# Kernel tuning notes

Hardware: AMD Instinct MI355X
Metric: run time of the kernel (lower is better)

## Reference

```python
import jax, jax.numpy as jnp
import numpy as np
import math

M, DIN, DTGT = 65536, 256, 256   # feature count and feature dims
S, SD_IN, SD_TGT = 64, 256, 256  # num_slots, in_slot_dim, tgt_slot_dim
ITERS = 3
H_IN = 128                        # mlp_in hidden (hardcoded 128 in source)
H_TGT = SD_TGT if SD_TGT > 128 else 128  # mlp_tgt hidden

ARGS = ["inputs", "target", "in_slots", "tgt_slots",
        "ln_in_g", "ln_in_b", "ln_tgt_g", "ln_tgt_b",
        "Wk", "bk", "Wv", "bv", "Wvt", "bvt",
        "ln_slots_g", "ln_slots_b", "Wq", "bq",
        "gru_in_Wih", "gru_in_Whh", "gru_in_bih", "gru_in_bhh",
        "gru_tgt_Wih", "gru_tgt_Whh", "gru_tgt_bih", "gru_tgt_bhh",
        "ln_mi_g", "ln_mi_b", "mi_W1", "mi_b1", "mi_W2", "mi_b2",
        "ln_mt_g", "ln_mt_b", "mt_W1", "mt_b1", "mt_W2", "mt_b2"]


def _ln(x, g, b):
    m = jnp.mean(x, axis=-1, keepdims=True)
    v = jnp.var(x, axis=-1, keepdims=True)
    return (x - m) * jax.lax.rsqrt(v + 1e-5) * g + b


def _gru(x, h, Wih, Whh, bih, bhh):
    # torch.nn.GRUCell semantics; Wih: (D, 3H), Whh: (H, 3H)
    H = h.shape[-1]
    gi = x @ Wih + bih
    gh = h @ Whh + bhh
    r = jax.nn.sigmoid(gi[:, :H] + gh[:, :H])
    z = jax.nn.sigmoid(gi[:, H:2 * H] + gh[:, H:2 * H])
    n = jnp.tanh(gi[:, 2 * H:] + r * gh[:, 2 * H:])
    return (1.0 - z) * n + z * h


def _forward(inputs, target, in_slots, tgt_slots,
             ln_in_g, ln_in_b, ln_tgt_g, ln_tgt_b,
             Wk, bk, Wv, bv, Wvt, bvt,
             ln_slots_g, ln_slots_b, Wq, bq,
             gru_in_Wih, gru_in_Whh, gru_in_bih, gru_in_bhh,
             gru_tgt_Wih, gru_tgt_Whh, gru_tgt_bih, gru_tgt_bhh,
             ln_mi_g, ln_mi_b, mi_W1, mi_b1, mi_W2, mi_b2,
             ln_mt_g, ln_mt_b, mt_W1, mt_b1, mt_W2, mt_b2):
    inputs_norm = _ln(inputs, ln_in_g, ln_in_b)          # [M, DIN]
    in_k = inputs_norm @ Wk + bk                          # [M, SD_IN]
    in_v = inputs_norm @ Wv + bv                          # [M, SD_IN]
    tgt_v = _ln(target, ln_tgt_g, ln_tgt_b) @ Wvt + bvt   # [M, SD_TGT]
    scale = 1.0 / math.sqrt(in_k.shape[1])
    attn = None
    for _ in range(ITERS):
        q = _ln(in_slots, ln_slots_g, ln_slots_b) @ Wq + bq   # [S, SD_IN]
        logits = (q @ in_k.T) * scale                          # [S, M]
        attn = jax.nn.softmax(logits, axis=0)                  # softmax over SLOTS (dim=0)
        in_up = attn @ in_v                                    # [S, SD_IN]
        tgt_up = attn @ tgt_v                                  # [S, SD_TGT]
        in_slots = _gru(in_up, in_slots, gru_in_Wih, gru_in_Whh, gru_in_bih, gru_in_bhh)
        tgt_slots = _gru(tgt_up, tgt_slots, gru_tgt_Wih, gru_tgt_Whh, gru_tgt_bih, gru_tgt_bhh)
        in_slots = in_slots + (jax.nn.relu(_ln(in_slots, ln_mi_g, ln_mi_b) @ mi_W1 + mi_b1) @ mi_W2 + mi_b2)
        tgt_slots = tgt_slots + (jax.nn.relu(_ln(tgt_slots, ln_mt_g, ln_mt_b) @ mt_W1 + mt_b1) @ mt_W2 + mt_b2)
    return (in_slots, tgt_slots, attn)


def setup_inputs() -> dict:
    key = jax.random.key(0)
    ks = iter(jax.random.split(key, 64))
    rn = lambda shape, s=1.0: jax.random.normal(next(ks), shape, dtype=jnp.float32) * s
    w = 0.02
    d = {
        "inputs": rn((M, DIN)),
        "target": rn((M, DTGT)),
        "in_slots": rn((S, SD_IN)),
        "tgt_slots": rn((S, SD_TGT)),
        "ln_in_g": jnp.ones((DIN,)), "ln_in_b": jnp.zeros((DIN,)),
        "ln_tgt_g": jnp.ones((DTGT,)), "ln_tgt_b": jnp.zeros((DTGT,)),
        "Wk": rn((DIN, SD_IN), w), "bk": jnp.zeros((SD_IN,)),
        "Wv": rn((DIN, SD_IN), w), "bv": jnp.zeros((SD_IN,)),
        "Wvt": rn((DTGT, SD_TGT), w), "bvt": jnp.zeros((SD_TGT,)),
        "ln_slots_g": jnp.ones((SD_IN,)), "ln_slots_b": jnp.zeros((SD_IN,)),
        "Wq": rn((SD_IN, SD_IN), w), "bq": jnp.zeros((SD_IN,)),
        "gru_in_Wih": rn((SD_IN, 3 * SD_IN), w), "gru_in_Whh": rn((SD_IN, 3 * SD_IN), w),
        "gru_in_bih": jnp.zeros((3 * SD_IN,)), "gru_in_bhh": jnp.zeros((3 * SD_IN,)),
        "gru_tgt_Wih": rn((SD_TGT, 3 * SD_TGT), w), "gru_tgt_Whh": rn((SD_TGT, 3 * SD_TGT), w),
        "gru_tgt_bih": jnp.zeros((3 * SD_TGT,)), "gru_tgt_bhh": jnp.zeros((3 * SD_TGT,)),
        "ln_mi_g": jnp.ones((SD_IN,)), "ln_mi_b": jnp.zeros((SD_IN,)),
        "mi_W1": rn((SD_IN, H_IN), w), "mi_b1": jnp.zeros((H_IN,)),
        "mi_W2": rn((H_IN, SD_IN), w), "mi_b2": jnp.zeros((SD_IN,)),
        "ln_mt_g": jnp.ones((SD_TGT,)), "ln_mt_b": jnp.zeros((SD_TGT,)),
        "mt_W1": rn((SD_TGT, H_TGT), w), "mt_b1": jnp.zeros((H_TGT,)),
        "mt_W2": rn((H_TGT, SD_TGT), w), "mt_b2": jnp.zeros((SD_TGT,)),
    }
    return {k: d[k] for k in ARGS}


def reference(inputs, target, in_slots, tgt_slots,
              ln_in_g, ln_in_b, ln_tgt_g, ln_tgt_b,
              Wk, bk, Wv, bv, Wvt, bvt,
              ln_slots_g, ln_slots_b, Wq, bq,
              gru_in_Wih, gru_in_Whh, gru_in_bih, gru_in_bhh,
              gru_tgt_Wih, gru_tgt_Whh, gru_tgt_bih, gru_tgt_bhh,
              ln_mi_g, ln_mi_b, mi_W1, mi_b1, mi_W2, mi_b2,
              ln_mt_g, ln_mt_b, mt_W1, mt_b1, mt_W2, mt_b2):
    return _forward(inputs, target, in_slots, tgt_slots,
                    ln_in_g, ln_in_b, ln_tgt_g, ln_tgt_b,
                    Wk, bk, Wv, bv, Wvt, bvt,
                    ln_slots_g, ln_slots_b, Wq, bq,
                    gru_in_Wih, gru_in_Whh, gru_in_bih, gru_in_bhh,
                    gru_tgt_Wih, gru_tgt_Whh, gru_tgt_bih, gru_tgt_bhh,
                    ln_mi_g, ln_mi_b, mi_W1, mi_b1, mi_W2, mi_b2,
                    ln_mt_g, ln_mt_b, mt_W1, mt_b1, mt_W2, mt_b2)
```

## Files before the change

kernel.cpp:

```cpp
#include <hip/hip_runtime.h>
#include <hip/hip_bf16.h>
#include <math.h>

typedef __bf16 bf16_t;
typedef __bf16 bf16x8 __attribute__((ext_vector_type(8)));
typedef __bf16 bf16x4 __attribute__((ext_vector_type(4)));
typedef float f32x4 __attribute__((ext_vector_type(4)));

#define DEVI __device__ __forceinline__

DEVI f32x4 mfma16(bf16x8 a, bf16x8 b, f32x4 c) {
  return __builtin_amdgcn_mfma_f32_16x16x32_bf16(a, b, c, 0, 0, 0);
}
DEVI bf16x8 ld8(const bf16_t* p) { return *reinterpret_cast<const bf16x8*>(p); }


struct WtArgs { const float* s0; const float* s1; const float* s2; const float* s3;
                const float* s4; const float* s5; const float* s6; const float* s7;
                const float* s8; const float* s9; const float* s10; const float* s11; };

__global__ __launch_bounds__(256) void k_wtrans(WtArgs A, bf16_t* __restrict__ wt,
                                                const float* __restrict__ g_in,
                                                const float* __restrict__ g_tgt) {
  constexpr int offs[12] = {0,65536,131072,196608,262144,458752,655360,851968,
                            1048576,1081344,1114112,1179648};
  constexpr int Ks[12]   = {256,256,256,256,256,256,256,256,256,128,256,256};
  constexpr int Ns[12]   = {256,256,256,256,768,768,768,768,128,256,256,256};
  const int m = blockIdx.y;
  const int K = Ks[m], N = Ns[m];
  const int tn = N >> 6;
  const int tile = blockIdx.x;
  if (tile >= (K >> 6) * tn) return;
  const int tk = tile / tn, tc = tile - tk * tn;
  const float* sp;
  switch (m) {
    case 0: sp = A.s0; break; case 1: sp = A.s1; break; case 2: sp = A.s2; break;
    case 3: sp = A.s3; break; case 4: sp = A.s4; break; case 5: sp = A.s5; break;
    case 6: sp = A.s6; break; case 7: sp = A.s7; break; case 8: sp = A.s8; break;
    case 9: sp = A.s9; break; case 10: sp = A.s10; break; default: sp = A.s11; break;
  }
  const float* gv = (m == 2) ? g_tgt : ((m < 2) ? g_in : nullptr);
  __shared__ float ts[64][65];
  const int t = threadIdx.x;
  const int k0 = tk * 64, n0 = tc * 64;
  {
    const int c = t & 63, rq = t >> 6;
    #pragma unroll
    for (int i = 0; i < 16; ++i) {
      const int r = rq * 16 + i;
      float val = sp[(size_t)(k0 + r) * N + n0 + c];
      if (gv) val *= gv[k0 + r];
      ts[r][c] = val;
    }
  }
  __syncthreads();
  bf16_t* dst = wt + offs[m];
  const int n_l = t & 63, kq = t >> 6;
  #pragma unroll
  for (int h = 0; h < 2; ++h) {
    const int k_l = kq * 16 + h * 8;
    bf16x8 pk;
    #pragma unroll
    for (int e = 0; e < 8; ++e) pk[e] = (bf16_t)ts[k_l + e][n_l];
    const int n_g = n0 + n_l, k_g = k0 + k_l;
    const int nt = n_g >> 4, kc = k_g >> 5;
    const int lane = (((k_g >> 3) & 3) << 4) + (n_g & 15);
    *reinterpret_cast<bf16x8*>(dst + (((size_t)(nt * (K >> 5) + kc)) << 9) + lane * 8) = pk;
  }
}

__global__ __launch_bounds__(256) void k_bias(
    const float* __restrict__ Wk, const float* __restrict__ Wv, const float* __restrict__ Wvt,
    const float* __restrict__ b_in, const float* __restrict__ b_tgt,
    const float* __restrict__ bk, const float* __restrict__ bv, const float* __restrict__ bvt,
    float* __restrict__ out) {
  const int which = blockIdx.x;
  const float* W = which == 0 ? Wk : (which == 1 ? Wv : Wvt);
  const float* bvec = which == 2 ? b_tgt : b_in;
  const float* bias = which == 0 ? bk : (which == 1 ? bv : bvt);
  const int n = threadIdx.x;
  float sum = bias[n];
  for (int k = 0; k < 256; ++k) sum += bvec[k] * W[(size_t)k * 256 + n];
  out[which * 256 + n] = sum;
}

__global__ __launch_bounds__(256) void k_init(const float* __restrict__ in_slots,
                                              const float* __restrict__ tgt_slots,
                                              float* __restrict__ h_f32,
                                              bf16_t* __restrict__ h_bf) {
  int idx = blockIdx.x * 256 + threadIdx.x;
  int side = idx >> 14, j = idx & 16383;
  int s = j >> 8, d = j & 255;
  float x = (side ? tgt_slots : in_slots)[j];
  h_f32[idx] = x;
  h_bf[side*16384 + (((s>>4)*8 + (d>>5))<<9) + ((d>>3)&3)*128 + (s&15)*8 + (d&7)] = (bf16_t)x;
}

__global__ __launch_bounds__(256) void k_phaseA(
    const float* __restrict__ inputs, const float* __restrict__ target,
    const bf16_t* __restrict__ wkF, const bf16_t* __restrict__ wvF, const bf16_t* __restrict__ wvtF,
    const float* __restrict__ bfold,
    bf16_t* __restrict__ in_kF, bf16_t* __restrict__ in_vF, bf16_t* __restrict__ tgt_vF) {
  const int side = blockIdx.y;
  const int t = threadIdx.x, l = t & 63, w = t >> 6;
  const int l16 = l & 15, l4 = l >> 4;
  const int mbase = blockIdx.x * 128 + w * 32;
  const float* src = side ? target : inputs;
  __shared__ __align__(16) bf16_t stg[4][2][512];

  bf16x8 A[2][8];
  #pragma unroll 1
  for (int mt = 0; mt < 2; ++mt) {
    const int row = mbase + mt*16 + l16;
    const float* rp = src + (size_t)row * 256 + l4 * 8;
    float4 xa[8], xb[8];
    #pragma unroll
    for (int j = 0; j < 8; ++j) {
      xa[j] = *reinterpret_cast<const float4*>(rp + j*32);
      xb[j] = *reinterpret_cast<const float4*>(rp + j*32 + 4);
    }
    float s1 = 0.f, s2 = 0.f;
    #pragma unroll
    for (int j = 0; j < 8; ++j) {
      s1 += xa[j].x + xa[j].y + xa[j].z + xa[j].w + xb[j].x + xb[j].y + xb[j].z + xb[j].w;
      s2 += xa[j].x*xa[j].x + xa[j].y*xa[j].y + xa[j].z*xa[j].z + xa[j].w*xa[j].w
          + xb[j].x*xb[j].x + xb[j].y*xb[j].y + xb[j].z*xb[j].z + xb[j].w*xb[j].w;
    }
    s1 += __shfl_xor(s1, 16); s1 += __shfl_xor(s1, 32);
    s2 += __shfl_xor(s2, 16); s2 += __shfl_xor(s2, 32);
    const float mean = s1 * (1.f/256.f);
    const float rstd = rsqrtf(s2 * (1.f/256.f) - mean*mean + 1e-5f);
    #pragma unroll
    for (int j = 0; j < 8; ++j) {
      bf16x8 pk;
      pk[0] = (bf16_t)((xa[j].x - mean) * rstd);
      pk[1] = (bf16_t)((xa[j].y - mean) * rstd);
      pk[2] = (bf16_t)((xa[j].z - mean) * rstd);
      pk[3] = (bf16_t)((xa[j].w - mean) * rstd);
      pk[4] = (bf16_t)((xb[j].x - mean) * rstd);
      pk[5] = (bf16_t)((xb[j].y - mean) * rstd);
      pk[6] = (bf16_t)((xb[j].z - mean) * rstd);
      pk[7] = (bf16_t)((xb[j].w - mean) * rstd);
      A[mt][j] = pk;
    }
  }

  const int mtg0 = mbase >> 4;
  const int mcg  = mbase >> 5;

  if (side == 0) {
    #pragma unroll 1
    for (int nt = 0; nt < 16; ++nt) {
      f32x4 a0 = {}, a1 = {};
      #pragma unroll
      for (int ks = 0; ks < 8; ++ks) {
        bf16x8 b = ld8(wkF + (((size_t)(nt*8 + ks)) << 9) + l*8);
        a0 = mfma16(A[0][ks], b, a0);
        a1 = mfma16(A[1][ks], b, a1);
      }
      const float bias = bfold[nt*16 + l16];
      const int half = (nt&1)*2 + (l16>>3);
      #pragma unroll
      for (int mt = 0; mt < 2; ++mt) {
        const f32x4 av = mt ? a1 : a0;
        bf16_t* sp = &stg[w][mt][half*128 + (l16&7)];
        #pragma unroll
        for (int rr = 0; rr < 4; ++rr)
          sp[(l4*4 + rr)*8] = (bf16_t)(av[rr] + bias);
      }
      if (nt & 1) {
        #pragma unroll
        for (int mt = 0; mt < 2; ++mt) {
          bf16x8 vv = *reinterpret_cast<const bf16x8*>(&stg[w][mt][l*8]);
          *reinterpret_cast<bf16x8*>(in_kF +
              (((size_t)((mtg0 + mt)*8 + (nt>>1))) << 9) + l*8) = vv;
        }
      }
    }
    #pragma unroll 1
    for (int nt = 0; nt < 16; ++nt) {
      f32x4 a0 = {}, a1 = {};
      #pragma unroll
      for (int ks = 0; ks < 8; ++ks) {
        bf16x8 b = ld8(wvF + (((size_t)(nt*8 + ks)) << 9) + l*8);
        a0 = mfma16(A[0][ks], b, a0);
        a1 = mfma16(A[1][ks], b, a1);
      }
      const float bias = bfold[256 + nt*16 + l16];
      #pragma unroll
      for (int mt = 0; mt < 2; ++mt) {
        const f32x4 av = mt ? a1 : a0;
        #pragma unroll
        for (int rr = 0; rr < 4; ++rr) {
          const int mlo = mt*16 + l4*4 + rr;
          stg[w][0][(mlo>>3)*128 + l16*8 + (mlo&7)] = (bf16_t)(av[rr] + bias);
        }
      }
      bf16x8 vv = *reinterpret_cast<const bf16x8*>(&stg[w][0][l*8]);
      *reinterpret_cast<bf16x8*>(in_vF + (((size_t)(nt*2048 + mcg)) << 9) + l*8) = vv;
    }
  } else {
    #pragma unroll 1
    for (int nt = 0; nt < 16; ++nt) {
      f32x4 a0 = {}, a1 = {};
      #pragma unroll
      for (int ks = 0; ks < 8; ++ks) {
        bf16x8 b = ld8(wvtF + (((size_t)(nt*8 + ks)) << 9) + l*8);
        a0 = mfma16(A[0][ks], b, a0);
        a1 = mfma16(A[1][ks], b, a1);
      }
      const float bias = bfold[512 + nt*16 + l16];
      #pragma unroll
      for (int mt = 0; mt < 2; ++mt) {
        const f32x4 av = mt ? a1 : a0;
        #pragma unroll
        for (int rr = 0; rr < 4; ++rr) {
          const int mlo = mt*16 + l4*4 + rr;
          stg[w][0][(mlo>>3)*128 + l16*8 + (mlo&7)] = (bf16_t)(av[rr] + bias);
        }
      }
      bf16x8 vv = *reinterpret_cast<const bf16x8*>(&stg[w][0][l*8]);
      *reinterpret_cast<bf16x8*>(tgt_vF + (((size_t)(nt*2048 + mcg)) << 9) + l*8) = vv;
    }
  }
}

__global__ __launch_bounds__(256) void k_q(
    const float* __restrict__ h_in,
    const float* __restrict__ ln_g, const float* __restrict__ ln_b,
    const bf16_t* __restrict__ wqF, const float* __restrict__ bq,
    bf16_t* __restrict__ q_bf) {
  __shared__ __align__(16) bf16_t anorm[64][264];
  const int t = threadIdx.x, l = t & 63, w = t >> 6;
  const float4 g4 = *reinterpret_cast<const float4*>(ln_g + l * 4);
  const float4 b4 = *reinterpret_cast<const float4*>(ln_b + l * 4);
  float4 v[16];
  #pragma unroll
  for (int i = 0; i < 16; ++i)
    v[i] = *reinterpret_cast<const float4*>(h_in + (size_t)(w*16 + i) * 256 + l * 4);
  #pragma unroll
  for (int i = 0; i < 16; ++i) {
    float s1 = v[i].x + v[i].y + v[i].z + v[i].w;
    float s2 = v[i].x*v[i].x + v[i].y*v[i].y + v[i].z*v[i].z + v[i].w*v[i].w;
    #pragma unroll
    for (int msk = 1; msk < 64; msk <<= 1) { s1 += __shfl_xor(s1, msk); s2 += __shfl_xor(s2, msk); }
    const float mean = s1 * (1.f/256.f);
    const float rstd = rsqrtf(s2 * (1.f/256.f) - mean*mean + 1e-5f);
    bf16x4 pk;
    pk[0] = (bf16_t)((v[i].x - mean) * rstd * g4.x + b4.x);
    pk[1] = (bf16_t)((v[i].y - mean) * rstd * g4.y + b4.y);
    pk[2] = (bf16_t)((v[i].z - mean) * rstd * g4.z + b4.z);
    pk[3] = (bf16_t)((v[i].w - mean) * rstd * g4.w + b4.w);
    *reinterpret_cast<bf16x4*>(&anorm[w*16 + i][l*4]) = pk;
  }
  __syncthreads();
  const int l16 = l & 15, l4 = l >> 4;
  f32x4 acc[4][4] = {};
  for (int ks = 0; ks < 8; ++ks) {
    const int k = ks*32 + l4*8;
    bf16x8 a[4], b[4];
    #pragma unroll
    for (int mi = 0; mi < 4; ++mi) a[mi] = ld8(&anorm[mi*16 + l16][k]);
    #pragma unroll
    for (int ni = 0; ni < 4; ++ni) b[ni] = ld8(wqF + (((size_t)((w*4 + ni)*8 + ks)) << 9) + l*8);
    #pragma unroll
    for (int mi = 0; mi < 4; ++mi)
      #pragma unroll
      for (int ni = 0; ni < 4; ++ni) acc[mi][ni] = mfma16(a[mi], b[ni], acc[mi][ni]);
  }
  #pragma unroll
  for (int mi = 0; mi < 4; ++mi)
    #pragma unroll
    for (int ni = 0; ni < 4; ++ni) {
      const int d = w*64 + ni*16 + l16;
      const float bias = bq[d];
      bf16_t* outp = q_bf + (((size_t)(mi*8 + w*2 + (ni>>1))) << 9) + ((ni&1)*2 + (l16>>3))*128 + (l16&7);
      #pragma unroll
      for (int rr = 0; rr < 4; ++rr)
        outp[(l4*4 + rr)*8] = (bf16_t)((acc[mi][ni][rr] + bias) * 0.0625f);
    }
}

__global__ __launch_bounds__(256) void k_logits(
    const bf16_t* __restrict__ q_bf, const bf16_t* __restrict__ in_kF,
    bf16_t* __restrict__ attnF, float* __restrict__ attn_f32, int write_f32) {
  __shared__ __align__(16) bf16_t stg[4][64][68];
  const int t = threadIdx.x, l = t & 63, w = t >> 6, l16 = l & 15, l4 = l >> 4;
  const int m0 = blockIdx.x * 256 + w * 64;
  f32x4 acc[4][4] = {};
  for (int ks = 0; ks < 8; ++ks) {
    bf16x8 a[4], b[4];
    #pragma unroll
    for (int mi = 0; mi < 4; ++mi) a[mi] = ld8(q_bf + (((size_t)(mi*8 + ks)) << 9) + l*8);
    #pragma unroll
    for (int ni = 0; ni < 4; ++ni)
      b[ni] = ld8(in_kF + (((size_t)((blockIdx.x*16 + w*4 + ni)*8 + ks)) << 9) + l*8);
    #pragma unroll
    for (int mi = 0; mi < 4; ++mi)
      #pragma unroll
      for (int ni = 0; ni < 4; ++ni) acc[mi][ni] = mfma16(a[mi], b[ni], acc[mi][ni]);
  }
  #pragma unroll
  for (int ni = 0; ni < 4; ++ni) {
    float mx = -3.0e38f;
    #pragma unroll
    for (int mi = 0; mi < 4; ++mi)
      #pragma unroll
      for (int rr = 0; rr < 4; ++rr) mx = fmaxf(mx, acc[mi][ni][rr]);
    mx = fmaxf(mx, __shfl_xor(mx, 16));
    mx = fmaxf(mx, __shfl_xor(mx, 32));
    float sm = 0.f;
    #pragma unroll
    for (int mi = 0; mi < 4; ++mi)
      #pragma unroll
      for (int rr = 0; rr < 4; ++rr) {
        float ev = __expf(acc[mi][ni][rr] - mx);
        acc[mi][ni][rr] = ev; sm += ev;
      }
    sm += __shfl_xor(sm, 16);
    sm += __shfl_xor(sm, 32);
    const float inv = 1.0f / sm;
    #pragma unroll
    for (int mi = 0; mi < 4; ++mi)
      #pragma unroll
      for (int rr = 0; rr < 4; ++rr) acc[mi][ni][rr] *= inv;
  }
  #pragma unroll
  for (int mi = 0; mi < 4; ++mi)
    #pragma unroll
    for (int ni = 0; ni < 4; ++ni)
      #pragma unroll
      for (int rr = 0; rr < 4; ++rr) {
        stg[w][mi*16 + l4*4 + rr][ni*16 + l16] = (bf16_t)acc[mi][ni][rr];
        if (write_f32) {
          const int s = mi*16 + l4*4 + rr;
          attn_f32[(size_t)s*65536 + (m0 + ni*16 + l16)] = acc[mi][ni][rr];
        }
      }
  #pragma unroll
  for (int mi = 0; mi < 4; ++mi)
    #pragma unroll
    for (int mc = 0; mc < 2; ++mc) {
      bf16x8 vv = *reinterpret_cast<const bf16x8*>(&stg[w][mi*16 + l16][mc*32 + l4*8]);
      *reinterpret_cast<bf16x8*>(attnF +
          ((((size_t)mi)*2048 + (blockIdx.x*8 + w*2 + mc)) << 9) + l*8) = vv;
    }
}

__global__ __launch_bounds__(256) void k_pv(
    const bf16_t* __restrict__ attnF,
    const bf16_t* __restrict__ in_vF, const bf16_t* __restrict__ tgt_vF,
    bf16_t* __restrict__ p_in, bf16_t* __restrict__ p_tgt) {
  const int c = blockIdx.x, side = blockIdx.y;
  const bf16_t* V = side ? tgt_vF : in_vF;
  bf16_t* P = side ? p_tgt : p_in;
  const int t = threadIdx.x, l = t & 63, w = t >> 6, l16 = l & 15, l4 = l >> 4;
  f32x4 acc[4][4] = {};
  for (int ks = 0; ks < 8; ++ks) {
    const size_t mc = (size_t)c*8 + ks;
    bf16x8 a[4], b[4];
    #pragma unroll
    for (int mi = 0; mi < 4; ++mi) a[mi] = ld8(attnF + ((((size_t)mi)*2048 + mc) << 9) + l*8);
    #pragma unroll
    for (int ni = 0; ni < 4; ++ni) b[ni] = ld8(V + ((((size_t)(w*4 + ni))*2048 + mc) << 9) + l*8);
    #pragma unroll
    for (int mi = 0; mi < 4; ++mi)
      #pragma unroll
      for (int ni = 0; ni < 4; ++ni) acc[mi][ni] = mfma16(a[mi], b[ni], acc[mi][ni]);
  }
  #pragma unroll
  for (int mi = 0; mi < 4; ++mi)
    #pragma unroll
    for (int ni = 0; ni < 4; ++ni) {
      const int d = w*64 + ni*16 + l16;
      #pragma unroll
      for (int rr = 0; rr < 4; ++rr) {
        const int s = mi*16 + l4*4 + rr;
        P[(size_t)c*16384 + s*256 + d] = (bf16_t)acc[mi][ni][rr];
      }
    }
}

__global__ __launch_bounds__(256) void k_pvred(
    const bf16_t* __restrict__ p_in, const bf16_t* __restrict__ p_tgt,
    bf16_t* __restrict__ upF) {
  const int b = blockIdx.x;
  const int side = b >> 6, s = b & 63;
  const int d = threadIdx.x;
  const bf16_t* P = (side ? p_tgt : p_in) + s*256 + d;
  float sum = 0.f;
  #pragma unroll 8
  for (int cc = 0; cc < 256; ++cc) sum += (float)P[(size_t)cc * 16384];
  upF[side*16384 + (((s>>4)*8 + (d>>5))<<9) + ((d>>3)&3)*128 + (s&15)*8 + (d&7)] = (bf16_t)sum;
}

__global__ __launch_bounds__(256) void k_gates(
    const bf16_t* __restrict__ upF, const bf16_t* __restrict__ h_bf,
    const bf16_t* __restrict__ wihF_in, const bf16_t* __restrict__ whhF_in,
    const bf16_t* __restrict__ wihF_tgt, const bf16_t* __restrict__ whhF_tgt,
    const float* __restrict__ bih_in, const float* __restrict__ bhh_in,
    const float* __restrict__ bih_tgt, const float* __restrict__ bhh_tgt,
    float* __restrict__ gi, float* __restrict__ gh) {
  const int nchunk = blockIdx.x, which = blockIdx.y, side = blockIdx.z;
  const bf16_t* Aop = (which ? h_bf : upF) + side*16384;
  const bf16_t* WF = side ? (which ? whhF_tgt : wihF_tgt) : (which ? whhF_in : wihF_in);
  const float* bias = side ? (which ? bhh_tgt : bih_tgt) : (which ? bhh_in : bih_in);
  float* out = (which ? gh : gi) + side*49152;
  const int t = threadIdx.x, l = t & 63, w = t >> 6, l16 = l & 15, l4 = l >> 4;
  const int n0 = nchunk*256 + w*64;
  f32x4 acc[4][4] = {};
  for (int ks = 0; ks < 8; ++ks) {
    bf16x8 a[4], b[4];
    #pragma unroll
    for (int mi = 0; mi < 4; ++mi) a[mi] = ld8(Aop + (((size_t)(mi*8 + ks)) << 9) + l*8);
    #pragma unroll
    for (int ni = 0; ni < 4; ++ni)
      b[ni] = ld8(WF + (((size_t)((nchunk*16 + w*4 + ni)*8 + ks)) << 9) + l*8);
    #pragma unroll
    for (int mi = 0; mi < 4; ++mi)
      #pragma unroll
      for (int ni = 0; ni < 4; ++ni) acc[mi][ni] = mfma16(a[mi], b[ni], acc[mi][ni]);
  }
  #pragma unroll
  for (int mi = 0; mi < 4; ++mi)
    #pragma unroll
    for (int ni = 0; ni < 4; ++ni) {
      const int n = n0 + ni*16 + l16;
      const float bb = bias[n];
      #pragma unroll
      for (int rr = 0; rr < 4; ++rr) {
        const int s = mi*16 + l4*4 + rr;
        out[(size_t)s*768 + n] = acc[mi][ni][rr] + bb;
      }
    }
}

__global__ __launch_bounds__(256) void k_gru_ln(
    const float* __restrict__ gi, const float* __restrict__ gh,
    const float* __restrict__ h_f32,
    const float* __restrict__ ln_mi_g, const float* __restrict__ ln_mi_b,
    const float* __restrict__ ln_mt_g, const float* __restrict__ ln_mt_b,
    float* __restrict__ hp_f32, bf16_t* __restrict__ hpnF) {
  const int s = blockIdx.x, side = blockIdx.y;
  const int d = threadIdx.x;
  const float* GI = gi + side*49152 + s*768;
  const float* GH = gh + side*49152 + s*768;
  const float hv = h_f32[side*16384 + s*256 + d];
  const float rg = 1.f / (1.f + __expf(-(GI[d] + GH[d])));
  const float zg = 1.f / (1.f + __expf(-(GI[256 + d] + GH[256 + d])));
  const float ng = tanhf(GI[512 + d] + rg * GH[512 + d]);
  const float hp = (1.f - zg) * ng + zg * hv;
  float a = hp, b2 = hp * hp;
  #pragma unroll
  for (int msk = 1; msk < 64; msk <<= 1) { a += __shfl_xor(a, msk); b2 += __shfl_xor(b2, msk); }
  __shared__ float reda[4], redb[4];
  const int w = d >> 6, lid = d & 63;
  if (lid == 0) { reda[w] = a; redb[w] = b2; }
  __syncthreads();
  const float S1 = reda[0] + reda[1] + reda[2] + reda[3];
  const float S2 = redb[0] + redb[1] + redb[2] + redb[3];
  const float mean = S1 * (1.f/256.f);
  const float rstd = rsqrtf(S2 * (1.f/256.f) - mean*mean + 1e-5f);
  const float* g = side ? ln_mt_g : ln_mi_g;
  const float* bb = side ? ln_mt_b : ln_mi_b;
  const float nv = (hp - mean) * rstd * g[d] + bb[d];
  hp_f32[side*16384 + s*256 + d] = hp;
  hpnF[side*16384 + (((s>>4)*8 + (d>>5))<<9) + ((d>>3)&3)*128 + (s&15)*8 + (d&7)] = (bf16_t)nv;
}

__global__ __launch_bounds__(256) void k_mlpq(
    const bf16_t* __restrict__ hpnF,
    const bf16_t* __restrict__ w1F_in, const bf16_t* __restrict__ w1F_tgt,
    const float* __restrict__ b1_in, const float* __restrict__ b1_tgt,
    const bf16_t* __restrict__ w2F_in, const bf16_t* __restrict__ w2F_tgt,
    const float* __restrict__ b2_in, const float* __restrict__ b2_tgt,
    const float* __restrict__ hp_f32,
    float* __restrict__ h_f32, bf16_t* __restrict__ h_bf, float* __restrict__ slots_out,
    const float* __restrict__ ln_sg, const float* __restrict__ ln_sb,
    const bf16_t* __restrict__ wqF, const float* __restrict__ bq,
    bf16_t* __restrict__ q_bf, int make_q) {
  const int side = blockIdx.x;
  __shared__ __align__(16) bf16_t hid[64][264];
  const int t = threadIdx.x, l = t & 63, w = t >> 6, l16 = l & 15, l4 = l >> 4;
  const int NH = side ? 256 : 128;
  {
    const bf16_t* Aop = hpnF + side*16384;
    const bf16_t* WF = side ? w1F_tgt : w1F_in;
    const float* b1 = side ? b1_tgt : b1_in;
    const int ntiles = NH >> 6;
    for (int nt = 0; nt < ntiles; ++nt) {
      const int n0 = w*(NH>>2) + nt*16;
      f32x4 acc[4] = {};
      for (int ks = 0; ks < 8; ++ks) {
        bf16x8 b = ld8(WF + (((size_t)((n0>>4)*8 + ks)) << 9) + l*8);
        #pragma unroll
        for (int mt = 0; mt < 4; ++mt)
          acc[mt] = mfma16(ld8(Aop + (((size_t)(mt*8 + ks)) << 9) + l*8), b, acc[mt]);
      }
      const float bb = b1[n0 + l16];
      #pragma unroll
      for (int mt = 0; mt < 4; ++mt)
        #pragma unroll
        for (int rr = 0; rr < 4; ++rr) {
          const int s = mt*16 + l4*4 + rr;
          hid[s][n0 + l16] = (bf16_t)fmaxf(acc[mt][rr] + bb, 0.f);
        }
    }
  }
  __syncthreads();
  {
    const bf16_t* WF = side ? w2F_tgt : w2F_in;
    const float* b2 = side ? b2_tgt : b2_in;
    const int ksteps = NH >> 5;
    #pragma unroll
    for (int nt = 0; nt < 4; ++nt) {
      const int n0 = w*64 + nt*16;
      f32x4 acc[4] = {};
      for (int ks = 0; ks < ksteps; ++ks) {
        const int k = ks*32 + l4*8;
        bf16x8 b = ld8(WF + (((size_t)((n0>>4)*ksteps + ks)) << 9) + l*8);
        #pragma unroll
        for (int mt = 0; mt < 4; ++mt)
          acc[mt] = mfma16(ld8(&hid[mt*16 + l16][k]), b, acc[mt]);
      }
      const int n = n0 + l16;
      const float bb = b2[n];
      #pragma unroll
      for (int mt = 0; mt < 4; ++mt)
        #pragma unroll
        for (int rr = 0; rr < 4; ++rr) {
          const int s = mt*16 + l4*4 + rr;
          const int idx = side*16384 + s*256 + n;
          const float val = acc[mt][rr] + bb + hp_f32[idx];
          h_f32[idx] = val;
          slots_out[idx] = val;
          h_bf[side*16384 + (((s>>4)*8 + (n>>5))<<9) + ((n>>3)&3)*128 + (s&15)*8 + (n&7)] = (bf16_t)val;
        }
    }
  }
  if (!make_q || side != 0) return;
  __syncthreads();
  {
    for (int i = 0; i < 16; ++i) {
      const int s = w*16 + i;
      float4 x = *reinterpret_cast<const float4*>(h_f32 + s*256 + 4*l);
      float a = x.x + x.y + x.z + x.w;
      float b2s = x.x*x.x + x.y*x.y + x.z*x.z + x.w*x.w;
      #pragma unroll
      for (int msk = 1; msk < 64; msk <<= 1) { a += __shfl_xor(a, msk); b2s += __shfl_xor(b2s, msk); }
      const float mean = a * (1.f/256.f);
      const float rstd = rsqrtf(b2s * (1.f/256.f) - mean*mean + 1e-5f);
      float4 g4 = *reinterpret_cast<const float4*>(ln_sg + 4*l);
      float4 bb4 = *reinterpret_cast<const float4*>(ln_sb + 4*l);
      bf16x4 pk;
      pk[0] = (bf16_t)((x.x - mean) * rstd * g4.x + bb4.x);
      pk[1] = (bf16_t)((x.y - mean) * rstd * g4.y + bb4.y);
      pk[2] = (bf16_t)((x.z - mean) * rstd * g4.z + bb4.z);
      pk[3] = (bf16_t)((x.w - mean) * rstd * g4.w + bb4.w);
      *reinterpret_cast<bf16x4*>(&hid[s][4*l]) = pk;
    }
  }
  __syncthreads();
  {
    #pragma unroll
    for (int nt = 0; nt < 4; ++nt) {
      const int n0 = w*64 + nt*16;
      f32x4 acc[4] = {};
      for (int ks = 0; ks < 8; ++ks) {
        const int k = ks*32 + l4*8;
        bf16x8 b = ld8(wqF + (((size_t)((n0>>4)*8 + ks)) << 9) + l*8);
        #pragma unroll
        for (int mt = 0; mt < 4; ++mt)
          acc[mt] = mfma16(ld8(&hid[mt*16 + l16][k]), b, acc[mt]);
      }
      const int d = n0 + l16;
      const float bb = bq[d];
      #pragma unroll
      for (int mt = 0; mt < 4; ++mt) {
        bf16_t* op = q_bf + (((size_t)(mt*8 + (d>>5))) << 9) + ((d>>3)&3)*128 + (d&7);
        #pragma unroll
        for (int rr = 0; rr < 4; ++rr)
          op[(l4*4 + rr)*8] = (bf16_t)((acc[mt][rr] + bb) * 0.0625f);
      }
    }
  }
}

extern "C" void kernel_launch(void* const* d_in, const int* in_sizes, int n_in,
                              void* d_out, int out_size, void* d_ws, size_t ws_size,
                              hipStream_t stream) {
  (void)in_sizes; (void)n_in; (void)out_size; (void)ws_size;
  const float* inputs     = (const float*)d_in[0];
  const float* target     = (const float*)d_in[1];
  const float* in_slots   = (const float*)d_in[2];
  const float* tgt_slots  = (const float*)d_in[3];
  const float* ln_in_g    = (const float*)d_in[4];
  const float* ln_in_b    = (const float*)d_in[5];
  const float* ln_tgt_g   = (const float*)d_in[6];
  const float* ln_tgt_b   = (const float*)d_in[7];
  const float* Wk  = (const float*)d_in[8];
  const float* bk  = (const float*)d_in[9];
  const float* Wv  = (const float*)d_in[10];
  const float* bv  = (const float*)d_in[11];
  const float* Wvt = (const float*)d_in[12];
  const float* bvt = (const float*)d_in[13];
  const float* ln_slots_g = (const float*)d_in[14];
  const float* ln_slots_b = (const float*)d_in[15];
  const float* Wq  = (const float*)d_in[16];
  const float* bq  = (const float*)d_in[17];
  const float* gru_in_Wih  = (const float*)d_in[18];
  const float* gru_in_Whh  = (const float*)d_in[19];
  const float* gru_in_bih  = (const float*)d_in[20];
  const float* gru_in_bhh  = (const float*)d_in[21];
  const float* gru_tgt_Wih = (const float*)d_in[22];
  const float* gru_tgt_Whh = (const float*)d_in[23];
  const float* gru_tgt_bih = (const float*)d_in[24];
  const float* gru_tgt_bhh = (const float*)d_in[25];
  const float* ln_mi_g = (const float*)d_in[26];
  const float* ln_mi_b = (const float*)d_in[27];
  const float* mi_W1 = (const float*)d_in[28];
  const float* mi_b1 = (const float*)d_in[29];
  const float* mi_W2 = (const float*)d_in[30];
  const float* mi_b2 = (const float*)d_in[31];
  const float* ln_mt_g = (const float*)d_in[32];
  const float* ln_mt_b = (const float*)d_in[33];
  const float* mt_W1 = (const float*)d_in[34];
  const float* mt_b1 = (const float*)d_in[35];
  const float* mt_W2 = (const float*)d_in[36];
  const float* mt_b2 = (const float*)d_in[37];

  char* ws = (char*)d_ws;
  bf16_t* wt      = (bf16_t*)(ws);
  bf16_t* in_kF   = (bf16_t*)(ws + 2490368ull);
  bf16_t* in_vF   = (bf16_t*)(ws + 36044800ull);
  bf16_t* tgt_vF  = (bf16_t*)(ws + 69599232ull);
  bf16_t* attnF   = (bf16_t*)(ws + 103153664ull);
  bf16_t* q_bf    = (bf16_t*)(ws + 111542272ull);
  bf16_t* h_bf    = (bf16_t*)(ws + 111575040ull);
  bf16_t* upF     = (bf16_t*)(ws + 111640576ull);
  bf16_t* hpnF    = (bf16_t*)(ws + 111673344ull);
  float*  h_f32   = (float*)(ws + 111706112ull);
  float*  hp_f32  = (float*)(ws + 111837184ull);
  float*  gi      = (float*)(ws + 111968256ull);
  float*  gh      = (float*)(ws + 112361472ull);
  bf16_t* p_in    = (bf16_t*)(ws + 112754688ull);
  bf16_t* p_tgt   = (bf16_t*)(ws + 121143296ull);
  float*  bfold   = (float*)(ws + 129531904ull);

  bf16_t* wkF = wt;
  bf16_t* wvF = wt + 65536;
  bf16_t* wvtF = wt + 131072;
  bf16_t* wqF = wt + 196608;
  bf16_t* wihF_in  = wt + 262144;
  bf16_t* whhF_in  = wt + 458752;
  bf16_t* wihF_tgt = wt + 655360;
  bf16_t* whhF_tgt = wt + 851968;
  bf16_t* w1F_in  = wt + 1048576;
  bf16_t* w2F_in  = wt + 1081344;
  bf16_t* w1F_tgt = wt + 1114112;
  bf16_t* w2F_tgt = wt + 1179648;

  float* attn_out = (float*)d_out + 32768;

  WtArgs wa = {Wk, Wv, Wvt, Wq, gru_in_Wih, gru_in_Whh, gru_tgt_Wih, gru_tgt_Whh,
               mi_W1, mi_W2, mt_W1, mt_W2};
  k_wtrans<<<dim3(48, 12), 256, 0, stream>>>(wa, wt, ln_in_g, ln_tgt_g);
  k_bias<<<3, 256, 0, stream>>>(Wk, Wv, Wvt, ln_in_b, ln_tgt_b, bk, bv, bvt, bfold);
  k_init<<<128, 256, 0, stream>>>(in_slots, tgt_slots, h_f32, h_bf);
  k_phaseA<<<dim3(512, 2), 256, 0, stream>>>(inputs, target,
      wkF, wvF, wvtF, bfold, in_kF, in_vF, tgt_vF);
  k_q<<<1, 256, 0, stream>>>(h_f32, ln_slots_g, ln_slots_b, wqF, bq, q_bf);

  for (int it = 0; it < 3; ++it) {
    k_logits<<<256, 256, 0, stream>>>(q_bf, in_kF, attnF, attn_out, it == 2 ? 1 : 0);
    k_pv<<<dim3(256, 2), 256, 0, stream>>>(attnF, in_vF, tgt_vF, p_in, p_tgt);
    k_pvred<<<128, 256, 0, stream>>>(p_in, p_tgt, upF);
    k_gates<<<dim3(3, 2, 2), 256, 0, stream>>>(upF, h_bf, wihF_in, whhF_in,
        wihF_tgt, whhF_tgt, gru_in_bih, gru_in_bhh, gru_tgt_bih, gru_tgt_bhh, gi, gh);
    k_gru_ln<<<dim3(64, 2), 256, 0, stream>>>(gi, gh, h_f32, ln_mi_g, ln_mi_b,
        ln_mt_g, ln_mt_b, hp_f32, hpnF);
    k_mlpq<<<2, 256, 0, stream>>>(hpnF, w1F_in, w1F_tgt, mi_b1, mt_b1,
        w2F_in, w2F_tgt, mi_b2, mt_b2, hp_f32, h_f32, h_bf, (float*)d_out,
        ln_slots_g, ln_slots_b, wqF, bq, q_bf, it < 2 ? 1 : 0);
  }
}
```

Measured before the change: 356.7 us.

## Fuse GRU gates, GRU/LN and MLP into one tail kernel; halve PV partial chunks

Merges the gate GEMMs, the GRU update with layernorm, and the MLP/q kernels into a single 2-block kernel per iteration. Intermediates (normalized hidden, hp) now live in shared memory instead of going through global memory. This removes two launches per iteration but runs the gate GEMMs on only 2 blocks instead of 12. Separately, k_pv now processes 16 K-chunks per block with half the grid, so k_pvred reduces over 128 partials instead of 256. The fused kernel also uses 128KB of static shared memory.

```diff
diff --git a/kernel.cpp b/kernel.cpp
--- a/kernel.cpp
+++ b/kernel.cpp
@@ -13,6 +13,7 @@
   return __builtin_amdgcn_mfma_f32_16x16x32_bf16(a, b, c, 0, 0, 0);
 }
 DEVI bf16x8 ld8(const bf16_t* p) { return *reinterpret_cast<const bf16x8*>(p); }
+DEVI float sigm(float x) { return 1.f / (1.f + __expf(-x)); }
 
 
 struct WtArgs { const float* s0; const float* s1; const float* s2; const float* s3;
@@ -356,8 +357,8 @@
   bf16_t* P = side ? p_tgt : p_in;
   const int t = threadIdx.x, l = t & 63, w = t >> 6, l16 = l & 15, l4 = l >> 4;
   f32x4 acc[4][4] = {};
-  for (int ks = 0; ks < 8; ++ks) {
-    const size_t mc = (size_t)c*8 + ks;
+  for (int ks = 0; ks < 16; ++ks) {
+    const size_t mc = (size_t)c*16 + ks;
     bf16x8 a[4], b[4];
     #pragma unroll
     for (int mi = 0; mi < 4; ++mi) a[mi] = ld8(attnF + ((((size_t)mi)*2048 + mc) << 9) + l*8);
@@ -390,120 +391,138 @@
   const bf16_t* P = (side ? p_tgt : p_in) + s*256 + d;
   float sum = 0.f;
   #pragma unroll 8
-  for (int cc = 0; cc < 256; ++cc) sum += (float)P[(size_t)cc * 16384];
+  for (int cc = 0; cc < 128; ++cc) sum += (float)P[(size_t)cc * 16384];
   upF[side*16384 + (((s>>4)*8 + (d>>5))<<9) + ((d>>3)&3)*128 + (s&15)*8 + (d&7)] = (bf16_t)sum;
 }
 
-__global__ __launch_bounds__(256) void k_gates(
-    const bf16_t* __restrict__ upF, const bf16_t* __restrict__ h_bf,
+__global__ __launch_bounds__(256) void k_tail(
+    const bf16_t* __restrict__ upF, bf16_t* __restrict__ h_bf,
     const bf16_t* __restrict__ wihF_in, const bf16_t* __restrict__ whhF_in,
     const bf16_t* __restrict__ wihF_tgt, const bf16_t* __restrict__ whhF_tgt,
     const float* __restrict__ bih_in, const float* __restrict__ bhh_in,
     const float* __restrict__ bih_tgt, const float* __restrict__ bhh_tgt,
-    float* __restrict__ gi, float* __restrict__ gh) {
-  const int nchunk = blockIdx.x, which = blockIdx.y, side = blockIdx.z;
-  const bf16_t* Aop = (which ? h_bf : upF) + side*16384;
-  const bf16_t* WF = side ? (which ? whhF_tgt : wihF_tgt) : (which ? whhF_in : wihF_in);
-  const float* bias = side ? (which ? bhh_tgt : bih_tgt) : (which ? bhh_in : bih_in);
-  float* out = (which ? gh : gi) + side*49152;
-  const int t = threadIdx.x, l = t & 63, w = t >> 6, l16 = l & 15, l4 = l >> 4;
-  const int n0 = nchunk*256 + w*64;
-  f32x4 acc[4][4] = {};
-  for (int ks = 0; ks < 8; ++ks) {
-    bf16x8 a[4], b[4];
-    #pragma unroll
-    for (int mi = 0; mi < 4; ++mi) a[mi] = ld8(Aop + (((size_t)(mi*8 + ks)) << 9) + l*8);
-    #pragma unroll
-    for (int ni = 0; ni < 4; ++ni)
-      b[ni] = ld8(WF + (((size_t)((nchunk*16 + w*4 + ni)*8 + ks)) << 9) + l*8);
-    #pragma unroll
-    for (int mi = 0; mi < 4; ++mi)
-      #pragma unroll
-      for (int ni = 0; ni < 4; ++ni) acc[mi][ni] = mfma16(a[mi], b[ni], acc[mi][ni]);
-  }
-  #pragma unroll
-  for (int mi = 0; mi < 4; ++mi)
-    #pragma unroll
-    for (int ni = 0; ni < 4; ++ni) {
-      const int n = n0 + ni*16 + l16;
-      const float bb = bias[n];
-      #pragma unroll
-      for (int rr = 0; rr < 4; ++rr) {
-        const int s = mi*16 + l4*4 + rr;
-        out[(size_t)s*768 + n] = acc[mi][ni][rr] + bb;
-      }
-    }
-}
-
-__global__ __launch_bounds__(256) void k_gru_ln(
-    const float* __restrict__ gi, const float* __restrict__ gh,
-    const float* __restrict__ h_f32,
+    float* __restrict__ gi, float* __restrict__ gh,
+    float* __restrict__ h_f32,
     const float* __restrict__ ln_mi_g, const float* __restrict__ ln_mi_b,
     const float* __restrict__ ln_mt_g, const float* __restrict__ ln_mt_b,
-    float* __restrict__ hp_f32, bf16_t* __restrict__ hpnF) {
-  const int s = blockIdx.x, side = blockIdx.y;
-  const int d = threadIdx.x;
-  const float* GI = gi + side*49152 + s*768;
-  const float* GH = gh + side*49152 + s*768;
-  const float hv = h_f32[side*16384 + s*256 + d];
-  const float rg = 1.f / (1.f + __expf(-(GI[d] + GH[d])));
-  const float zg = 1.f / (1.f + __expf(-(GI[256 + d] + GH[256 + d])));
-  const float ng = tanhf(GI[512 + d] + rg * GH[512 + d]);
-  const float hp = (1.f - zg) * ng + zg * hv;
-  float a = hp, b2 = hp * hp;
-  #pragma unroll
-  for (int msk = 1; msk < 64; msk <<= 1) { a += __shfl_xor(a, msk); b2 += __shfl_xor(b2, msk); }
-  __shared__ float reda[4], redb[4];
-  const int w = d >> 6, lid = d & 63;
-  if (lid == 0) { reda[w] = a; redb[w] = b2; }
-  __syncthreads();
-  const float S1 = reda[0] + reda[1] + reda[2] + reda[3];
-  const float S2 = redb[0] + redb[1] + redb[2] + redb[3];
-  const float mean = S1 * (1.f/256.f);
-  const float rstd = rsqrtf(S2 * (1.f/256.f) - mean*mean + 1e-5f);
-  const float* g = side ? ln_mt_g : ln_mi_g;
-  const float* bb = side ? ln_mt_b : ln_mi_b;
-  const float nv = (hp - mean) * rstd * g[d] + bb[d];
-  hp_f32[side*16384 + s*256 + d] = hp;
-  hpnF[side*16384 + (((s>>4)*8 + (d>>5))<<9) + ((d>>3)&3)*128 + (s&15)*8 + (d&7)] = (bf16_t)nv;
-}
-
-__global__ __launch_bounds__(256) void k_mlpq(
-    const bf16_t* __restrict__ hpnF,
     const bf16_t* __restrict__ w1F_in, const bf16_t* __restrict__ w1F_tgt,
     const float* __restrict__ b1_in, const float* __restrict__ b1_tgt,
     const bf16_t* __restrict__ w2F_in, const bf16_t* __restrict__ w2F_tgt,
     const float* __restrict__ b2_in, const float* __restrict__ b2_tgt,
-    const float* __restrict__ hp_f32,
-    float* __restrict__ h_f32, bf16_t* __restrict__ h_bf, float* __restrict__ slots_out,
+    float* __restrict__ slots_out,
     const float* __restrict__ ln_sg, const float* __restrict__ ln_sb,
     const bf16_t* __restrict__ wqF, const float* __restrict__ bq,
     bf16_t* __restrict__ q_bf, int make_q) {
   const int side = blockIdx.x;
-  __shared__ __align__(16) bf16_t hid[64][264];
+  __shared__ __align__(16) char smem[131072];
+  bf16_t* hpnL = (bf16_t*)smem;
+  bf16_t* hidL = (bf16_t*)(smem + 32768);
+  float*  hpL  = (float*)(smem + 65536);
+  bf16_t (*hidRM)[264] = (bf16_t(*)[264])(smem + 65536);
+
   const int t = threadIdx.x, l = t & 63, w = t >> 6, l16 = l & 15, l4 = l >> 4;
   const int NH = side ? 256 : 128;
+
   {
-    const bf16_t* Aop = hpnF + side*16384;
+    #pragma unroll 1
+    for (int which = 0; which < 2; ++which) {
+      const bf16_t* Aop = (which ? h_bf : upF) + side*16384;
+      const bf16_t* WF = side ? (which ? whhF_tgt : wihF_tgt) : (which ? whhF_in : wihF_in);
+      const float* bias = side ? (which ? bhh_tgt : bih_tgt) : (which ? bhh_in : bih_in);
+      float* out = (which ? gh : gi) + side*49152;
+      #pragma unroll 1
+      for (int nt12 = 0; nt12 < 12; ++nt12) {
+        const int ntg = w*12 + nt12;
+        f32x4 acc[4] = {};
+        #pragma unroll
+        for (int ks = 0; ks < 8; ++ks) {
+          bf16x8 b = ld8(WF + (((size_t)(ntg*8 + ks)) << 9) + l*8);
+          #pragma unroll
+          for (int mi = 0; mi < 4; ++mi)
+            acc[mi] = mfma16(ld8(Aop + (((size_t)(mi*8 + ks)) << 9) + l*8), b, acc[mi]);
+        }
+        const int n = ntg*16 + l16;
+        const float bb = bias[n];
+        #pragma unroll
+        for (int mi = 0; mi < 4; ++mi)
+          #pragma unroll
+          for (int rr = 0; rr < 4; ++rr)
+            out[(size_t)(mi*16 + l4*4 + rr)*768 + n] = acc[mi][rr] + bb;
+      }
+    }
+  }
+  __syncthreads();
+  {
+    const float* GIb = gi + side*49152;
+    const float* GHb = gh + side*49152;
+    const float* g = side ? ln_mt_g : ln_mi_g;
+    const float* bb = side ? ln_mt_b : ln_mi_b;
+    const float4 g4 = *reinterpret_cast<const float4*>(g + l*4);
+    const float4 b4 = *reinterpret_cast<const float4*>(bb + l*4);
+    const int d = l*4;
+    #pragma unroll 1
+    for (int i = 0; i < 16; ++i) {
+      const int r = w*16 + i;
+      float4 gi1 = *reinterpret_cast<const float4*>(GIb + r*768 + d);
+      float4 gi2 = *reinterpret_cast<const float4*>(GIb + r*768 + 256 + d);
+      float4 gi3 = *reinterpret_cast<const float4*>(GIb + r*768 + 512 + d);
+      float4 gh1 = *reinterpret_cast<const float4*>(GHb + r*768 + d);
+      float4 gh2 = *reinterpret_cast<const float4*>(GHb + r*768 + 256 + d);
+      float4 gh3 = *reinterpret_cast<const float4*>(GHb + r*768 + 512 + d);
+      float4 hv = *reinterpret_cast<const float4*>(h_f32 + side*16384 + r*256 + d);
+      float4 hp;
+      {
+        float rg, zg, ng;
+        rg = sigm(gi1.x + gh1.x); zg = sigm(gi2.x + gh2.x);
+        ng = tanhf(gi3.x + rg * gh3.x); hp.x = (1.f - zg) * ng + zg * hv.x;
+        rg = sigm(gi1.y + gh1.y); zg = sigm(gi2.y + gh2.y);
+        ng = tanhf(gi3.y + rg * gh3.y); hp.y = (1.f - zg) * ng + zg * hv.y;
+        rg = sigm(gi1.z + gh1.z); zg = sigm(gi2.z + gh2.z);
+        ng = tanhf(gi3.z + rg * gh3.z); hp.z = (1.f - zg) * ng + zg * hv.z;
+        rg = sigm(gi1.w + gh1.w); zg = sigm(gi2.w + gh2.w);
+        ng = tanhf(gi3.w + rg * gh3.w); hp.w = (1.f - zg) * ng + zg * hv.w;
+      }
+      float s1 = hp.x + hp.y + hp.z + hp.w;
+      float s2 = hp.x*hp.x + hp.y*hp.y + hp.z*hp.z + hp.w*hp.w;
+      #pragma unroll
+      for (int msk = 1; msk < 64; msk <<= 1) { s1 += __shfl_xor(s1, msk); s2 += __shfl_xor(s2, msk); }
+      const float mean = s1 * (1.f/256.f);
+      const float rstd = rsqrtf(s2 * (1.f/256.f) - mean*mean + 1e-5f);
+      bf16x4 pk;
+      pk[0] = (bf16_t)((hp.x - mean) * rstd * g4.x + b4.x);
+      pk[1] = (bf16_t)((hp.y - mean) * rstd * g4.y + b4.y);
+      pk[2] = (bf16_t)((hp.z - mean) * rstd * g4.z + b4.z);
+      pk[3] = (bf16_t)((hp.w - mean) * rstd * g4.w + b4.w);
+      *reinterpret_cast<bf16x4*>(hpnL + (((r>>4)*8 + (d>>5))<<9)
+          + ((d>>3)&3)*128 + (r&15)*8 + (d&7)) = pk;
+      *reinterpret_cast<float4*>(hpL + r*256 + d) = hp;
+    }
+  }
+  __syncthreads();
+  {
     const bf16_t* WF = side ? w1F_tgt : w1F_in;
     const float* b1 = side ? b1_tgt : b1_in;
     const int ntiles = NH >> 6;
+    #pragma unroll 1
     for (int nt = 0; nt < ntiles; ++nt) {
       const int n0 = w*(NH>>2) + nt*16;
       f32x4 acc[4] = {};
+      #pragma unroll
       for (int ks = 0; ks < 8; ++ks) {
         bf16x8 b = ld8(WF + (((size_t)((n0>>4)*8 + ks)) << 9) + l*8);
         #pragma unroll
         for (int mt = 0; mt < 4; ++mt)
-          acc[mt] = mfma16(ld8(Aop + (((size_t)(mt*8 + ks)) << 9) + l*8), b, acc[mt]);
-      }
-      const float bb = b1[n0 + l16];
+          acc[mt] = mfma16(ld8(hpnL + ((mt*8 + ks) << 9) + l*8), b, acc[mt]);
+      }
+      const int n = n0 + l16;
+      const float bb = b1[n];
       #pragma unroll
       for (int mt = 0; mt < 4; ++mt)
         #pragma unroll
         for (int rr = 0; rr < 4; ++rr) {
           const int s = mt*16 + l4*4 + rr;
-          hid[s][n0 + l16] = (bf16_t)fmaxf(acc[mt][rr] + bb, 0.f);
+          hidL[(((s>>4)*(NH>>5) + (n>>5))<<9) + ((n>>3)&3)*128 + (s&15)*8 + (n&7)]
+              = (bf16_t)fmaxf(acc[mt][rr] + bb, 0.f);
         }
     }
   }
@@ -512,16 +531,15 @@
     const bf16_t* WF = side ? w2F_tgt : w2F_in;
     const float* b2 = side ? b2_tgt : b2_in;
     const int ksteps = NH >> 5;
-    #pragma unroll
+    #pragma unroll 1
     for (int nt = 0; nt < 4; ++nt) {
       const int n0 = w*64 + nt*16;
       f32x4 acc[4] = {};
       for (int ks = 0; ks < ksteps; ++ks) {
-        const int k = ks*32 + l4*8;
         bf16x8 b = ld8(WF + (((size_t)((n0>>4)*ksteps + ks)) << 9) + l*8);
         #pragma unroll
         for (int mt = 0; mt < 4; ++mt)
-          acc[mt] = mfma16(ld8(&hid[mt*16 + l16][k]), b, acc[mt]);
+          acc[mt] = mfma16(ld8(hidL + ((mt*ksteps + ks) << 9) + l*8), b, acc[mt]);
       }
       const int n = n0 + l16;
       const float bb = b2[n];
@@ -531,7 +549,7 @@
         for (int rr = 0; rr < 4; ++rr) {
           const int s = mt*16 + l4*4 + rr;
           const int idx = side*16384 + s*256 + n;
-          const float val = acc[mt][rr] + bb + hp_f32[idx];
+          const float val = acc[mt][rr] + bb + hpL[s*256 + n];
           h_f32[idx] = val;
           slots_out[idx] = val;
           h_bf[side*16384 + (((s>>4)*8 + (n>>5))<<9) + ((n>>3)&3)*128 + (s&15)*8 + (n&7)] = (bf16_t)val;
@@ -541,6 +559,7 @@
   if (!make_q || side != 0) return;
   __syncthreads();
   {
+    #pragma unroll 1
     for (int i = 0; i < 16; ++i) {
       const int s = w*16 + i;
       float4 x = *reinterpret_cast<const float4*>(h_f32 + s*256 + 4*l);
@@ -557,12 +576,12 @@
       pk[1] = (bf16_t)((x.y - mean) * rstd * g4.y + bb4.y);
       pk[2] = (bf16_t)((x.z - mean) * rstd * g4.z + bb4.z);
       pk[3] = (bf16_t)((x.w - mean) * rstd * g4.w + bb4.w);
-      *reinterpret_cast<bf16x4*>(&hid[s][4*l]) = pk;
+      *reinterpret_cast<bf16x4*>(&hidRM[s][4*l]) = pk;
     }
   }
   __syncthreads();
   {
-    #pragma unroll
+    #pragma unroll 1
     for (int nt = 0; nt < 4; ++nt) {
       const int n0 = w*64 + nt*16;
       f32x4 acc[4] = {};
@@ -571,7 +590,7 @@
         bf16x8 b = ld8(wqF + (((size_t)((n0>>4)*8 + ks)) << 9) + l*8);
         #pragma unroll
         for (int mt = 0; mt < 4; ++mt)
-          acc[mt] = mfma16(ld8(&hid[mt*16 + l16][k]), b, acc[mt]);
+          acc[mt] = mfma16(ld8(&hidRM[mt*16 + l16][k]), b, acc[mt]);
       }
       const int d = n0 + l16;
       const float bb = bq[d];
@@ -638,9 +657,7 @@
   bf16_t* q_bf    = (bf16_t*)(ws + 111542272ull);
   bf16_t* h_bf    = (bf16_t*)(ws + 111575040ull);
   bf16_t* upF     = (bf16_t*)(ws + 111640576ull);
-  bf16_t* hpnF    = (bf16_t*)(ws + 111673344ull);
   float*  h_f32   = (float*)(ws + 111706112ull);
-  float*  hp_f32  = (float*)(ws + 111837184ull);
   float*  gi      = (float*)(ws + 111968256ull);
   float*  gh      = (float*)(ws + 112361472ull);
   bf16_t* p_in    = (bf16_t*)(ws + 112754688ull);
@@ -673,14 +690,12 @@
 
   for (int it = 0; it < 3; ++it) {
     k_logits<<<256, 256, 0, stream>>>(q_bf, in_kF, attnF, attn_out, it == 2 ? 1 : 0);
-    k_pv<<<dim3(256, 2), 256, 0, stream>>>(attnF, in_vF, tgt_vF, p_in, p_tgt);
+    k_pv<<<dim3(128, 2), 256, 0, stream>>>(attnF, in_vF, tgt_vF, p_in, p_tgt);
     k_pvred<<<128, 256, 0, stream>>>(p_in, p_tgt, upF);
-    k_gates<<<dim3(3, 2, 2), 256, 0, stream>>>(upF, h_bf, wihF_in, whhF_in,
-        wihF_tgt, whhF_tgt, gru_in_bih, gru_in_bhh, gru_tgt_bih, gru_tgt_bhh, gi, gh);
-    k_gru_ln<<<dim3(64, 2), 256, 0, stream>>>(gi, gh, h_f32, ln_mi_g, ln_mi_b,
-        ln_mt_g, ln_mt_b, hp_f32, hpnF);
-    k_mlpq<<<2, 256, 0, stream>>>(hpnF, w1F_in, w1F_tgt, mi_b1, mt_b1,
-        w2F_in, w2F_tgt, mi_b2, mt_b2, hp_f32, h_f32, h_bf, (float*)d_out,
-        ln_slots_g, ln_slots_b, wqF, bq, q_bf, it < 2 ? 1 : 0);
-  }
-}
+    k_tail<<<2, 256, 0, stream>>>(upF, h_bf, wihF_in, whhF_in, wihF_tgt, whhF_tgt,
+        gru_in_bih, gru_in_bhh, gru_tgt_bih, gru_tgt_bhh, gi, gh, h_f32,
+        ln_mi_g, ln_mi_b, ln_mt_g, ln_mt_b,
+        w1F_in, w1F_tgt, mi_b1, mt_b1, w2F_in, w2F_tgt, mi_b2, mt_b2,
+        (float*)d_out, ln_slots_g, ln_slots_b, wqF, bq, q_bf, it < 2 ? 1 : 0);
+  }
+}
```

Result: slower. 467.2 us (+31.0%).
